# Performance work log

Measured on AMD Instinct MI355X. Metric: run time of the kernel, lower is better.

Reference implementation:

```python
import jax, jax.numpy as jnp
import numpy as np

B, N, DIM = 8, 512, 768
H, DH = 12, 64
INNER = H * DH
MLP = 3072
DEPTH = 4
EPS = 1e-5
LS = 0.1  # LayerScale init_eps for depth <= 18


def _ln(x, scale):
    # flax LayerNorm(use_bias=False): (x-mean)/sqrt(var+eps) * scale
    mu = jnp.mean(x, axis=-1, keepdims=True)
    var = jnp.mean(jnp.square(x - mu), axis=-1, keepdims=True)
    return (x - mu) * jax.lax.rsqrt(var + EPS) * scale


def setup_inputs() -> dict:
    key = jax.random.key(0)
    ks = jax.random.split(key, 13)
    s = 0.02
    inp = {
        "x": jax.random.normal(ks[0], (B, N, DIM), jnp.float32),
        "ln1": jnp.ones((DEPTH, DIM), jnp.float32),
        "Wq": jax.random.normal(ks[1], (DEPTH, DIM, INNER), jnp.float32) * s,
        "Wkv": jax.random.normal(ks[2], (DEPTH, DIM, 2 * INNER), jnp.float32) * s,
        "mix_pre": jax.random.normal(ks[3], (DEPTH, H, H), jnp.float32) * 0.1,
        "mix_post": jax.random.normal(ks[4], (DEPTH, H, H), jnp.float32) * 0.1,
        "Wo": jax.random.normal(ks[5], (DEPTH, INNER, DIM), jnp.float32) * s,
        "bo": jnp.zeros((DEPTH, DIM), jnp.float32),
        "ln2": jnp.ones((DEPTH, DIM), jnp.float32),
        "W1": jax.random.normal(ks[6], (DEPTH, DIM, MLP), jnp.float32) * s,
        "b1": jnp.zeros((DEPTH, MLP), jnp.float32),
        "W2": jax.random.normal(ks[7], (DEPTH, MLP, DIM), jnp.float32) * s,
        "b2": jnp.zeros((DEPTH, DIM), jnp.float32),
    }
    return inp


def _block(x, p):
    ln1, Wq, Wkv, mp, mq, Wo, bo, ln2, W1, b1, W2, b2 = p
    scale = DH ** -0.5
    h = _ln(x, ln1)
    q = h @ Wq                                  # [b,n,inner]
    kv = h @ Wkv
    k, v = jnp.split(kv, 2, axis=-1)
    def to_heads(t):
        return t.reshape(B, N, H, DH).transpose(0, 2, 1, 3)  # b h n d
    q, k, v = to_heads(q), to_heads(k), to_heads(v)
    dots = jnp.einsum('bhid,bhjd->bhij', q, k) * scale
    dots = jnp.einsum('bhij,hg->bgij', dots, mp)   # talking-heads pre-softmax
    attn = jax.nn.softmax(dots, axis=-1)
    attn = jnp.einsum('bhij,hg->bgij', attn, mq)   # talking-heads post-softmax
    o = jnp.einsum('bhij,bhjd->bhid', attn, v)
    o = o.transpose(0, 2, 1, 3).reshape(B, N, INNER)
    x = (o @ Wo + bo) * LS + x
    h2 = _ln(x, ln2)
    x = ((jax.nn.gelu(h2 @ W1 + b1) @ W2) + b2) * LS + x
    return x, None


def reference(x, ln1, Wq, Wkv, mix_pre, mix_post, Wo, bo, ln2, W1, b1, W2, b2):
    params = (ln1, Wq, Wkv, mix_pre, mix_post, Wo, bo, ln2, W1, b1, W2, b2)
    out, _ = jax.lax.scan(_block, x, params)
    return out
```

## Files before the change

kernel.cpp:

```cpp
#include <hip/hip_runtime.h>


#define LSCALE 0.1f

typedef __bf16 bf16;
typedef __bf16 bf16x8 __attribute__((ext_vector_type(8)));
typedef __bf16 bf16x4 __attribute__((ext_vector_type(4)));
typedef unsigned short ushort4v __attribute__((ext_vector_type(4)));
typedef float  f32x4  __attribute__((ext_vector_type(4)));

__device__ __forceinline__ void g2l16(const void* g, void* l) {
    __builtin_amdgcn_global_load_lds(
        (const __attribute__((address_space(1))) void*)g,
        (__attribute__((address_space(3))) void*)l, 16, 0, 0);
}

template<int EPI, bool PLANA = false>
__global__ __launch_bounds__(256, 2)
void gemm_bt(const bf16* __restrict__ A, int lda, long saz1, long saz2,
             const bf16* __restrict__ Bt, int ldb, long sbz1, long sbz2,
             void* __restrict__ Cv, int ldc, long scz1, long scz2,
             int M, int N, int K, int zmod,
             const float* __restrict__ bias, float scale)
{
    __shared__ __align__(16) char smem[35840];
    bf16* As = (bf16*)smem;
    bf16* Bs = (bf16*)(smem + 16384);
    bf16* Cs = (bf16*)smem;

    const int z  = blockIdx.z;
    const int z1 = z / zmod, z2 = z - z1 * zmod;
    const bf16* Ab = A  + saz1 * (long)z1 + saz2 * (long)z2;
    const bf16* Bb = Bt + sbz1 * (long)z1 + sbz2 * (long)z2;

    const int m0 = blockIdx.x * 128, n0 = blockIdx.y * 128;
    const int tid = threadIdx.x, w = tid >> 6, l = tid & 63;
    const int wr = (w >> 1) * 64, wc = (w & 1) * 64;
    const int lr = l & 15, lq = l >> 4;
    const int srow = l >> 2, scol8 = (l & 3) * 8;

    long abase = 0;
    if constexpr (PLANA)
        abase = (long)(m0 >> 9) * 393216 + (long)((m0 & 511) + w * 32) * 64;

    f32x4 acc[4][4];
#pragma unroll
    for (int i = 0; i < 4; i++)
#pragma unroll
        for (int j = 0; j < 4; j++)
#pragma unroll
            for (int r = 0; r < 4; r++) acc[i][j][r] = 0.f;

    for (int k0 = 0; k0 < K; k0 += 64) {
        const bf16* Ag;
        int ldaa;
        if constexpr (PLANA) {
            Ag = Ab + abase + ((long)(k0 >> 6)) * 32768;
            ldaa = 64;
        } else {
            Ag = Ab + (long)(m0 + w * 32) * lda + k0;
            ldaa = lda;
        }
        const bf16* Bg = Bb + (long)(n0 + w * 32) * ldb + k0;
        g2l16(Ag + (long)srow * ldaa + scol8,             As + w * 1024);
        g2l16(Ag + (long)(srow + 16) * ldaa + scol8,      As + w * 1024 + 512);
        g2l16(Ag + (long)srow * ldaa + 32 + scol8,        As + 4096 + w * 1024);
        g2l16(Ag + (long)(srow + 16) * ldaa + 32 + scol8, As + 4096 + w * 1024 + 512);
        g2l16(Bg + (long)srow * ldb + scol8,             Bs + w * 1024);
        g2l16(Bg + (long)(srow + 16) * ldb + scol8,      Bs + w * 1024 + 512);
        g2l16(Bg + (long)srow * ldb + 32 + scol8,        Bs + 4096 + w * 1024);
        g2l16(Bg + (long)(srow + 16) * ldb + 32 + scol8, Bs + 4096 + w * 1024 + 512);
        __syncthreads();

#pragma unroll
        for (int hh = 0; hh < 2; hh++) {
            bf16x8 fa[4], fb[4];
#pragma unroll
            for (int i = 0; i < 4; i++)
                fa[i] = *(const bf16x8*)(As + hh * 4096 + (wr + i * 16 + lr) * 32 + lq * 8);
#pragma unroll
            for (int i = 0; i < 4; i++)
                fb[i] = *(const bf16x8*)(Bs + hh * 4096 + (wc + i * 16 + lr) * 32 + lq * 8);
#pragma unroll
            for (int mi = 0; mi < 4; mi++)
#pragma unroll
                for (int ni = 0; ni < 4; ni++)
                    acc[mi][ni] = __builtin_amdgcn_mfma_f32_16x16x32_bf16(
                        fa[mi], fb[ni], acc[mi][ni], 0, 0, 0);
        }
        __syncthreads();
    }

#pragma unroll
    for (int ni = 0; ni < 4; ni++) {
        const int col = wc + ni * 16 + lr;
        float bv = 0.f;
        if (EPI == 1) bv = bias[n0 + col];
#pragma unroll
        for (int mi = 0; mi < 4; mi++) {
#pragma unroll
            for (int r = 0; r < 4; r++) {
                const int row = wr + mi * 16 + lq * 4 + r;
                float v = acc[mi][ni][r];
                if (EPI == 0) {
                    v *= scale;
                } else if (EPI == 1) {
                    const float xx = v + bv;
                    const float u  = 0.7978845608f * (xx + 0.044715f * xx * xx * xx);
                    const float th = 1.f - 2.f / (__expf(2.f * u) + 1.f);
                    v = 0.5f * xx * (1.f + th);
                }
                Cs[row * 136 + col] = (bf16)v;
            }
        }
    }
    __syncthreads();

    const long cb = scz1 * (long)z1 + scz2 * (long)z2;
    const int rrow = tid >> 4, cg = tid & 15;
#pragma unroll
    for (int p = 0; p < 8; p++) {
        const int row = p * 16 + rrow;
        const bf16x8 v = *(const bf16x8*)(Cs + row * 136 + cg * 8);
        *(bf16x8*)((bf16*)Cv + cb + (long)(m0 + row) * ldc + n0 + cg * 8) = v;
    }
}

template<int PLANO>
__global__ __launch_bounds__(256, 4)
void gemm_av(const bf16* __restrict__ S, const bf16* __restrict__ qkvc,
             bf16* __restrict__ oc)
{
    __shared__ __align__(16) char av_smem[9728];
    bf16* As  = (bf16*)av_smem;
    bf16* Bst = (bf16*)(av_smem + 4096);
    bf16* Cs  = (bf16*)av_smem;

    const int z = blockIdx.y, b = z / 12, g = z - b * 12;
    const bf16* Ab = S + (long)z * 262144;
    const bf16* Bb = qkvc + (long)b * 1179648 + 1536 + g * 64;

    const int i0 = blockIdx.x * 64;
    const int tid = threadIdx.x, w = tid >> 6, l = tid & 63;
    const int lr = l & 15, lq = l >> 4;
    const int srow = l >> 2, scol8 = (l & 3) * 8;
    const int kp = tid >> 4, dq = tid & 15;
    const int kcol = ((((kp >> 2) ^ ((dq >> 1) & 3)) << 3) | ((kp & 3) << 1));

    f32x4 acc[4];
#pragma unroll
    for (int j = 0; j < 4; j++)
#pragma unroll
        for (int r = 0; r < 4; r++) acc[j][r] = 0.f;

    unsigned short* Bw = (unsigned short*)Bst;

    for (int k0 = 0; k0 < 512; k0 += 32) {
        const bf16* Ag = Ab + (long)(i0 + w * 16) * 512 + k0;
        g2l16(Ag + (long)srow * 512 + scol8, As + w * 512);

        const bf16* Bg = Bb + (long)(k0 + 2 * kp) * 2304 + dq * 4;
        ushort4v u0 = *(const ushort4v*)(Bg);
        ushort4v u1 = *(const ushort4v*)(Bg + 2304);
#pragma unroll
        for (int r = 0; r < 4; r++) {
            unsigned p = (unsigned)u0[r] | ((unsigned)u1[r] << 16);
            *(unsigned*)(Bw + (dq * 4 + r) * 40 + kcol) = p;
        }
        __syncthreads();

        bf16x8 fa = *(const bf16x8*)(As + (w * 16 + lr) * 32 + lq * 8);
        bf16x8 fb[4];
#pragma unroll
        for (int i = 0; i < 4; i++) {
            const int d = i * 16 + lr;
            fb[i] = *(const bf16x8*)(Bst + d * 40 + ((lq ^ ((d >> 3) & 3)) << 3));
        }
#pragma unroll
        for (int ni = 0; ni < 4; ni++)
            acc[ni] = __builtin_amdgcn_mfma_f32_16x16x32_bf16(
                fa, fb[ni], acc[ni], 0, 0, 0);
        __syncthreads();
    }

    if constexpr (PLANO) {
#pragma unroll
        for (int ni = 0; ni < 4; ni++)
#pragma unroll
            for (int r = 0; r < 4; r++)
                Cs[(w * 16 + lq * 4 + r) * 68 + ni * 16 + lr] = (bf16)acc[ni][r];
        __syncthreads();
        const int rr = tid >> 2, c16 = (tid & 3) * 16;
        bf16* orow = oc + ((long)z * 512 + i0 + rr) * 64 + c16;
        *(bf16x8*)(orow)     = *(const bf16x8*)(Cs + rr * 68 + c16);
        *(bf16x8*)(orow + 8) = *(const bf16x8*)(Cs + rr * 68 + c16 + 8);
    } else {
        bf16* Cb = oc + (long)b * 1179648 + g * 64;
#pragma unroll
        for (int ni = 0; ni < 4; ni++) {
            const int gc = ni * 16 + lr;
#pragma unroll
            for (int r = 0; r < 4; r++) {
                const int gr = i0 + w * 16 + lq * 4 + r;
                Cb[(long)gr * 2304 + gc] = (bf16)acc[ni][r];
            }
        }
    }
}

__global__ __launch_bounds__(256)
void tconv_k(const float* __restrict__ in, bf16* __restrict__ out,
             int K, int N)
{
    __shared__ float t[32][33];
    const int n0 = blockIdx.x * 32, k0 = blockIdx.y * 32;
    const int x = threadIdx.x, y = threadIdx.y;
#pragma unroll
    for (int yy = 0; yy < 4; yy++)
        t[y + yy * 8][x] = in[(long)(k0 + y + yy * 8) * N + n0 + x];
    __syncthreads();
#pragma unroll
    for (int yy = 0; yy < 4; yy++)
        out[(long)(n0 + y + yy * 8) * K + k0 + x] = (bf16)t[x][y + yy * 8];
}

__global__ __launch_bounds__(256)
void tconv_all(const float* __restrict__ Wq, const float* __restrict__ Wkv,
               const float* __restrict__ Wo, const float* __restrict__ W1,
               const float* __restrict__ W2, bf16* __restrict__ WtAll)
{
    __shared__ float st[128][65];
    const int L = blockIdx.y;
    bf16* WtL = WtAll + (long)L * 7077888;
    int bx = blockIdx.x;
    const float* src; bf16* dst; int K, N, ntn;
    if (bx < 72) {
        src = Wq + (long)L * 589824;   dst = WtL;            K = 768;  N = 768;  ntn = 12;
    } else if (bx < 216) {
        bx -= 72;
        src = Wkv + (long)L * 1179648; dst = WtL + 589824;   K = 768;  N = 1536; ntn = 24;
    } else if (bx < 288) {
        bx -= 216;
        src = Wo + (long)L * 589824;   dst = WtL + 1769472;  K = 768;  N = 768;  ntn = 12;
    } else if (bx < 576) {
        bx -= 288;
        src = W1 + (long)L * 2359296;  dst = WtL + 2359296;  K = 768;  N = 3072; ntn = 48;
    } else {
        bx -= 576;
        src = W2 + (long)L * 2359296;  dst = WtL + 4718592;  K = 3072; N = 768;  ntn = 12;
    }
    const int n0 = (bx % ntn) * 64, k0 = (bx / ntn) * 128;
    const int t = threadIdx.x;
    const int rr = t >> 1, cb = (t & 1) * 32;
    f32x4 v[8];
#pragma unroll
    for (int q = 0; q < 8; q++)
        v[q] = *(const f32x4*)(src + (long)(k0 + rr) * N + n0 + cb + 4 * q);
#pragma unroll
    for (int q = 0; q < 8; q++)
#pragma unroll
        for (int j = 0; j < 4; j++)
            st[rr][cb + 4 * q + j] = v[q][j];
    __syncthreads();
    const int kb = (t & 15) * 8;
#pragma unroll
    for (int p = 0; p < 4; p++) {
        const int n = p * 16 + (t >> 4);
        bf16x8 o;
#pragma unroll
        for (int e = 0; e < 8; e++) o[e] = (bf16)st[kb + e][n];
        *(bf16x8*)(dst + (long)(n0 + n) * K + k0 + kb) = o;
    }
}

__global__ __launch_bounds__(256)
void lnres_k(float* __restrict__ xf, const bf16* __restrict__ P0,
             const bf16* __restrict__ P1, const float* __restrict__ bias,
             const float* __restrict__ gam, bf16* __restrict__ out,
             const float* __restrict__ src)
{
    const int row = blockIdx.x, t = threadIdx.x;
    float* xr = xf + (long)row * 768;
    float v[3];
#pragma unroll
    for (int i = 0; i < 3; i++) {
        const int c = t + i * 256;
        float xv;
        if (src) {
            xv = src[(long)row * 768 + c];
            xr[c] = xv;
        } else if (P0) {
            xv = xr[c] + LSCALE * ((float)P0[(long)row * 768 + c] +
                                   (float)P1[(long)row * 768 + c] + bias[c]);
            xr[c] = xv;
        } else {
            xv = xr[c];
        }
        v[i] = xv;
    }
    float s  = v[0] + v[1] + v[2];
    float ss = v[0] * v[0] + v[1] * v[1] + v[2] * v[2];
#pragma unroll
    for (int off = 32; off; off >>= 1) {
        s  += __shfl_xor(s, off);
        ss += __shfl_xor(ss, off);
    }
    __shared__ float ps[4], pss[4];
    const int wv = t >> 6, l = t & 63;
    if (l == 0) { ps[wv] = s; pss[wv] = ss; }
    __syncthreads();
    s  = ps[0] + ps[1] + ps[2] + ps[3];
    ss = pss[0] + pss[1] + pss[2] + pss[3];
    const float mu = s * (1.f / 768.f);
    const float rs = rsqrtf(ss * (1.f / 768.f) - mu * mu + 1e-5f);
    bf16* orow = out + (long)row * 768;
#pragma unroll
    for (int i = 0; i < 3; i++) {
        const int c = t + i * 256;
        orow[c] = (bf16)((v[i] - mu) * rs * gam[c]);
    }
}

__global__ __launch_bounds__(256)
void outres_k(const float* __restrict__ xf, const bf16* __restrict__ P0,
              const bf16* __restrict__ P1, const float* __restrict__ bias,
              float* __restrict__ out)
{
    const long i4 = ((long)blockIdx.x * 256 + threadIdx.x) * 4;
    const int c = (int)(i4 % 768);
    const f32x4 xv = *(const f32x4*)(xf + i4);
    const bf16x4 p0 = *(const bf16x4*)(P0 + i4);
    const bf16x4 p1 = *(const bf16x4*)(P1 + i4);
    const f32x4 bv = *(const f32x4*)(bias + c);
    f32x4 o;
#pragma unroll
    for (int e = 0; e < 4; e++)
        o[e] = xv[e] + LSCALE * ((float)p0[e] + (float)p1[e] + bv[e]);
    *(f32x4*)(out + i4) = o;
}

__global__ __launch_bounds__(256)
void mixsm_k(bf16* __restrict__ S, const float* __restrict__ mp,
             const float* __restrict__ mq)
{
    __shared__ float buf[12][512];
    __shared__ float rds[12];
    const int b = blockIdx.y, i = blockIdx.x, t = threadIdx.x;
    bf16* Sb = S + ((long)b * 12 * 512 + i) * 512;

    float s0[12], s1[12];
#pragma unroll
    for (int h = 0; h < 12; h++) {
        union { unsigned u; bf16 v[2]; } p;
        p.u = *(const unsigned*)(Sb + (long)h * 262144 + 2 * t);
        s0[h] = (float)p.v[0];
        s1[h] = (float)p.v[1];
    }
#pragma unroll
    for (int g = 0; g < 12; g++) {
        float a0 = 0.f, a1 = 0.f;
#pragma unroll
        for (int h = 0; h < 12; h++) {
            const float m = mp[h * 12 + g];
            a0 += s0[h] * m;
            a1 += s1[h] * m;
        }
        *(float2*)(&buf[g][2 * t]) = make_float2(a0, a1);
    }
    __syncthreads();

    const int wv = t >> 6, l = t & 63;
    for (int g = wv; g < 12; g += 4) {
        float mx = -3.0e38f;
#pragma unroll
        for (int k = 0; k < 8; k++) mx = fmaxf(mx, buf[g][l + 64 * k]);
#pragma unroll
        for (int off = 32; off; off >>= 1) mx = fmaxf(mx, __shfl_xor(mx, off));
        float sm = 0.f;
#pragma unroll
        for (int k = 0; k < 8; k++) {
            const float e = __expf(buf[g][l + 64 * k] - mx);
            buf[g][l + 64 * k] = e;
            sm += e;
        }
#pragma unroll
        for (int off = 32; off; off >>= 1) sm += __shfl_xor(sm, off);
        if (l == 0) rds[g] = 1.f / sm;
    }
    __syncthreads();

    float e0[12], e1[12];
#pragma unroll
    for (int h = 0; h < 12; h++) {
        const float2 ee = *(const float2*)(&buf[h][2 * t]);
        const float rd = rds[h];
        e0[h] = ee.x * rd;
        e1[h] = ee.y * rd;
    }
#pragma unroll
    for (int g = 0; g < 12; g++) {
        float a0 = 0.f, a1 = 0.f;
#pragma unroll
        for (int h = 0; h < 12; h++) {
            const float m = mq[h * 12 + g];
            a0 += e0[h] * m;
            a1 += e1[h] * m;
        }
        union { unsigned u; bf16 v[2]; } p;
        p.v[0] = (bf16)a0;
        p.v[1] = (bf16)a1;
        *(unsigned*)(Sb + (long)g * 262144 + 2 * t) = p.u;
    }
}

extern "C" void kernel_launch(void* const* d_in, const int* in_sizes, int n_in,
                              void* d_out, int out_size, void* d_ws, size_t ws_size,
                              hipStream_t stream)
{
    (void)in_sizes; (void)n_in; (void)out_size;
    const float* x   = (const float*)d_in[0];
    const float* ln1 = (const float*)d_in[1];
    const float* Wq  = (const float*)d_in[2];
    const float* Wkv = (const float*)d_in[3];
    const float* mp  = (const float*)d_in[4];
    const float* mq  = (const float*)d_in[5];
    const float* Wo  = (const float*)d_in[6];
    const float* bo  = (const float*)d_in[7];
    const float* ln2 = (const float*)d_in[8];
    const float* W1  = (const float*)d_in[9];
    const float* b1  = (const float*)d_in[10];
    const float* W2  = (const float*)d_in[11];
    const float* b2  = (const float*)d_in[12];

    char* ws = (char*)d_ws;
    float* xf  = (float*)(ws);
    bf16* h    = (bf16*)(ws + 12582912);
    bf16* qkv  = (bf16*)(ws + 18874368);
    bf16* S    = (bf16*)(ws + 37748736);
    bf16* mid  = S;
    bf16* P0   = h;
    bf16* P1w2 = qkv;
    bf16* P1wo = S;
    const long P1W2_OFF = 3145728;
    const long P1WO_OFF = 12582912;

    const dim3 tb(32, 8);

    if (ws_size >= 150994944ull) {
        bf16* WtAll = (bf16*)(ws + 88080384);
        bf16* oP    = (bf16*)(ws + 144703488);

        tconv_all<<<dim3(864, 4), 256, 0, stream>>>(Wq, Wkv, Wo, W1, W2, WtAll);

        for (int L = 0; L < 4; L++) {
            bf16* WtL = WtAll + (long)L * 7077888;

            if (L == 0)
                lnres_k<<<4096, 256, 0, stream>>>(xf, nullptr, nullptr, nullptr,
                                                  ln1 + L * 768, h, x);
            else
                lnres_k<<<4096, 256, 0, stream>>>(xf, P0, P1w2, b2 + (L - 1) * 768,
                                                  ln1 + L * 768, h, nullptr);

            gemm_bt<0><<<dim3(32, 18, 1), 256, 0, stream>>>(
                h, 768, 0, 0, WtL, 768, 0, 0,
                qkv, 2304, 0, 0, 4096, 2304, 768, 1, nullptr, 1.f);

            gemm_bt<0><<<dim3(4, 4, 96), 256, 0, stream>>>(
                qkv,       2304, 1179648, 64,
                qkv + 768, 2304, 1179648, 64,
                S,          512, 3145728, 262144,
                512, 512, 64, 12, nullptr, 0.125f);

            mixsm_k<<<dim3(512, 8), 256, 0, stream>>>(S, mp + L * 144, mq + L * 144);

            gemm_av<1><<<dim3(8, 96), 256, 0, stream>>>(S, qkv, oP);

            gemm_bt<4, true><<<dim3(32, 6, 2), 256, 0, stream>>>(
                oP, 64, 0, 196608, WtL + 1769472, 768, 0, 384,
                P0, 768, 0, P1WO_OFF, 4096, 768, 384, 2, nullptr, 1.f);

            lnres_k<<<4096, 256, 0, stream>>>(xf, P0, P1wo, bo + L * 768,
                                              ln2 + L * 768, h, nullptr);

            gemm_bt<1><<<dim3(32, 24, 1), 256, 0, stream>>>(
                h, 768, 0, 0, WtL + 2359296, 768, 0, 0,
                mid, 3072, 0, 0, 4096, 3072, 768, 1, b1 + L * 3072, 1.f);

            gemm_bt<4><<<dim3(32, 6, 2), 256, 0, stream>>>(
                mid, 3072, 0, 1536, WtL + 4718592, 3072, 0, 1536,
                P0, 768, 0, P1W2_OFF, 4096, 768, 1536, 2, nullptr, 1.f);
        }
    } else {
        bf16* Wt = (bf16*)(ws + 62914560);

        for (int L = 0; L < 4; L++) {
            tconv_k<<<dim3(24, 24), tb, 0, stream>>>(Wq + (long)L * 589824, Wt, 768, 768);
            tconv_k<<<dim3(48, 24), tb, 0, stream>>>(Wkv + (long)L * 1179648, Wt + 589824, 768, 1536);

            if (L == 0)
                lnres_k<<<4096, 256, 0, stream>>>(xf, nullptr, nullptr, nullptr,
                                                  ln1 + L * 768, h, x);
            else
                lnres_k<<<4096, 256, 0, stream>>>(xf, P0, P1w2, b2 + (L - 1) * 768,
                                                  ln1 + L * 768, h, nullptr);

            gemm_bt<0><<<dim3(32, 18, 1), 256, 0, stream>>>(
                h, 768, 0, 0, Wt, 768, 0, 0,
                qkv, 2304, 0, 0, 4096, 2304, 768, 1, nullptr, 1.f);

            for (int c = 0; c < 2; c++) {
                const long qb = (long)c * 4718592;
                gemm_bt<0><<<dim3(4, 4, 48), 256, 0, stream>>>(
                    qkv + qb,       2304, 1179648, 64,
                    qkv + 768 + qb, 2304, 1179648, 64,
                    S,               512, 3145728, 262144,
                    512, 512, 64, 12, nullptr, 0.125f);

                mixsm_k<<<dim3(512, 4), 256, 0, stream>>>(S, mp + L * 144, mq + L * 144);

                gemm_av<0><<<dim3(8, 48), 256, 0, stream>>>(S, qkv + qb, qkv + qb);
            }

            tconv_k<<<dim3(24, 24), tb, 0, stream>>>(Wo + (long)L * 589824, Wt, 768, 768);
            gemm_bt<4><<<dim3(32, 6, 2), 256, 0, stream>>>(
                qkv, 2304, 0, 384, Wt, 768, 0, 384,
                P0, 768, 0, P1WO_OFF, 4096, 768, 384, 2, nullptr, 1.f);

            lnres_k<<<4096, 256, 0, stream>>>(xf, P0, P1wo, bo + L * 768,
                                              ln2 + L * 768, h, nullptr);

            tconv_k<<<dim3(96, 24), tb, 0, stream>>>(W1 + (long)L * 2359296, Wt, 768, 3072);
            gemm_bt<1><<<dim3(32, 24, 1), 256, 0, stream>>>(
                h, 768, 0, 0, Wt, 768, 0, 0,
                mid, 3072, 0, 0, 4096, 3072, 768, 1, b1 + L * 3072, 1.f);

            tconv_k<<<dim3(24, 96), tb, 0, stream>>>(W2 + (long)L * 2359296, Wt, 3072, 768);
            gemm_bt<4><<<dim3(32, 6, 2), 256, 0, stream>>>(
                mid, 3072, 0, 1536, Wt, 3072, 0, 1536,
                P0, 768, 0, P1W2_OFF, 4096, 768, 1536, 2, nullptr, 1.f);
        }
    }

    outres_k<<<3072, 256, 0, stream>>>(xf, P0, P1w2, b2 + 3 * 768, (float*)d_out);
}
```

Before: 902.1 us.

## Fuse weight transpose with first LayerNorm; register-resident talking-heads softmax per wave

Merges the up-front weight transpose/bf16 conversion with the layer-0 input copy and LayerNorm into one launch, using smaller 64x64 transpose tiles and more blocks. Rewrites the talking-heads mix+softmax kernel so each wave owns one full query row: values stay in registers, reductions use wave shuffles only, and the LDS buffer and block barriers are gone. Each thread now loads and stores 16-byte vectors, with a quarter as many blocks. The cost is much higher register pressure (a 12x8 float accumulator per thread), which may cut occupancy or cause spills, and the one-pass variance formula is slightly less numerically robust.

```diff
diff --git a/kernel.cpp b/kernel.cpp
--- a/kernel.cpp
+++ b/kernel.cpp
@@ -225,51 +225,90 @@
 }
 
 __global__ __launch_bounds__(256)
-void tconv_all(const float* __restrict__ Wq, const float* __restrict__ Wkv,
-               const float* __restrict__ Wo, const float* __restrict__ W1,
-               const float* __restrict__ W2, bf16* __restrict__ WtAll)
-{
-    __shared__ float st[128][65];
-    const int L = blockIdx.y;
-    bf16* WtL = WtAll + (long)L * 7077888;
-    int bx = blockIdx.x;
-    const float* src; bf16* dst; int K, N, ntn;
-    if (bx < 72) {
-        src = Wq + (long)L * 589824;   dst = WtL;            K = 768;  N = 768;  ntn = 12;
-    } else if (bx < 216) {
-        bx -= 72;
-        src = Wkv + (long)L * 1179648; dst = WtL + 589824;   K = 768;  N = 1536; ntn = 24;
-    } else if (bx < 288) {
-        bx -= 216;
-        src = Wo + (long)L * 589824;   dst = WtL + 1769472;  K = 768;  N = 768;  ntn = 12;
-    } else if (bx < 576) {
-        bx -= 288;
-        src = W1 + (long)L * 2359296;  dst = WtL + 2359296;  K = 768;  N = 3072; ntn = 48;
+void pre_k(const float* __restrict__ Wq, const float* __restrict__ Wkv,
+           const float* __restrict__ Wo, const float* __restrict__ W1,
+           const float* __restrict__ W2, bf16* __restrict__ WtAll,
+           const float* __restrict__ x, float* __restrict__ xf,
+           const float* __restrict__ gam, bf16* __restrict__ hout)
+{
+    __shared__ __align__(16) char pmem[16640];
+    const int bxg = blockIdx.x;
+    const int t = threadIdx.x;
+    if (bxg < 6912) {
+        float (*st)[65] = (float(*)[65])pmem;
+        const int L = bxg / 1728;
+        int bx = bxg - L * 1728;
+        bf16* WtL = WtAll + (long)L * 7077888;
+        const float* src; bf16* dst; int K, N, ntn;
+        if (bx < 144) {
+            src = Wq + (long)L * 589824;   dst = WtL;            K = 768;  N = 768;  ntn = 12;
+        } else if (bx < 432) {
+            bx -= 144;
+            src = Wkv + (long)L * 1179648; dst = WtL + 589824;   K = 768;  N = 1536; ntn = 24;
+        } else if (bx < 576) {
+            bx -= 432;
+            src = Wo + (long)L * 589824;   dst = WtL + 1769472;  K = 768;  N = 768;  ntn = 12;
+        } else if (bx < 1152) {
+            bx -= 576;
+            src = W1 + (long)L * 2359296;  dst = WtL + 2359296;  K = 768;  N = 3072; ntn = 48;
+        } else {
+            bx -= 1152;
+            src = W2 + (long)L * 2359296;  dst = WtL + 4718592;  K = 3072; N = 768;  ntn = 12;
+        }
+        const int n0 = (bx % ntn) * 64, k0 = (bx / ntn) * 64;
+        const int r = t >> 4, c4 = (t & 15) * 4;
+#pragma unroll
+        for (int rr = 0; rr < 4; rr++) {
+            const f32x4 v = *(const f32x4*)(src + (long)(k0 + r + rr * 16) * N + n0 + c4);
+            st[r + rr * 16][c4 + 0] = v[0];
+            st[r + rr * 16][c4 + 1] = v[1];
+            st[r + rr * 16][c4 + 2] = v[2];
+            st[r + rr * 16][c4 + 3] = v[3];
+        }
+        __syncthreads();
+        const int kc = (t & 7) * 8;
+#pragma unroll
+        for (int p = 0; p < 2; p++) {
+            const int n = p * 32 + (t >> 3);
+            bf16x8 o;
+#pragma unroll
+            for (int e = 0; e < 8; e++) o[e] = (bf16)st[kc + e][n];
+            *(bf16x8*)(dst + (long)(n0 + n) * K + k0 + kc) = o;
+        }
     } else {
-        bx -= 576;
-        src = W2 + (long)L * 2359296;  dst = WtL + 4718592;  K = 3072; N = 768;  ntn = 12;
-    }
-    const int n0 = (bx % ntn) * 64, k0 = (bx / ntn) * 128;
-    const int t = threadIdx.x;
-    const int rr = t >> 1, cb = (t & 1) * 32;
-    f32x4 v[8];
-#pragma unroll
-    for (int q = 0; q < 8; q++)
-        v[q] = *(const f32x4*)(src + (long)(k0 + rr) * N + n0 + cb + 4 * q);
-#pragma unroll
-    for (int q = 0; q < 8; q++)
-#pragma unroll
-        for (int j = 0; j < 4; j++)
-            st[rr][cb + 4 * q + j] = v[q][j];
-    __syncthreads();
-    const int kb = (t & 15) * 8;
-#pragma unroll
-    for (int p = 0; p < 4; p++) {
-        const int n = p * 16 + (t >> 4);
-        bf16x8 o;
-#pragma unroll
-        for (int e = 0; e < 8; e++) o[e] = (bf16)st[kb + e][n];
-        *(bf16x8*)(dst + (long)(n0 + n) * K + k0 + kb) = o;
+        const int row = bxg - 6912;
+        float* ps  = (float*)pmem;
+        float* pss = (float*)pmem + 4;
+        const float* xin = x + (long)row * 768;
+        float* xr = xf + (long)row * 768;
+        float v[3];
+#pragma unroll
+        for (int i = 0; i < 3; i++) {
+            const int c = t + i * 256;
+            const float xv = xin[c];
+            xr[c] = xv;
+            v[i] = xv;
+        }
+        float s  = v[0] + v[1] + v[2];
+        float ss = v[0] * v[0] + v[1] * v[1] + v[2] * v[2];
+#pragma unroll
+        for (int off = 32; off; off >>= 1) {
+            s  += __shfl_xor(s, off);
+            ss += __shfl_xor(ss, off);
+        }
+        const int wv = t >> 6, l = t & 63;
+        if (l == 0) { ps[wv] = s; pss[wv] = ss; }
+        __syncthreads();
+        s  = ps[0] + ps[1] + ps[2] + ps[3];
+        ss = pss[0] + pss[1] + pss[2] + pss[3];
+        const float mu = s * (1.f / 768.f);
+        const float rs = rsqrtf(ss * (1.f / 768.f) - mu * mu + 1e-5f);
+        bf16* orow = hout + (long)row * 768;
+#pragma unroll
+        for (int i = 0; i < 3; i++) {
+            const int c = t + i * 256;
+            orow[c] = (bf16)((v[i] - mu) * rs * gam[c]);
+        }
     }
 }
 
@@ -343,73 +382,75 @@
 void mixsm_k(bf16* __restrict__ S, const float* __restrict__ mp,
              const float* __restrict__ mq)
 {
-    __shared__ float buf[12][512];
-    __shared__ float rds[12];
-    const int b = blockIdx.y, i = blockIdx.x, t = threadIdx.x;
-    bf16* Sb = S + ((long)b * 12 * 512 + i) * 512;
-
-    float s0[12], s1[12];
+    const int b = blockIdx.y, i4 = blockIdx.x, t = threadIdx.x;
+    const int w = t >> 6, l = t & 63;
+    const int row = i4 * 4 + w;
+    bf16* Sb = S + ((long)b * 12 * 512 + row) * 512 + l * 8;
+
+    float a[12][8];
+#pragma unroll
+    for (int g = 0; g < 12; g++)
+#pragma unroll
+        for (int e = 0; e < 8; e++) a[g][e] = 0.f;
+
 #pragma unroll
     for (int h = 0; h < 12; h++) {
-        union { unsigned u; bf16 v[2]; } p;
-        p.u = *(const unsigned*)(Sb + (long)h * 262144 + 2 * t);
-        s0[h] = (float)p.v[0];
-        s1[h] = (float)p.v[1];
-    }
+        const bf16x8 sv = *(const bf16x8*)(Sb + (long)h * 262144);
+        float f[8];
+#pragma unroll
+        for (int e = 0; e < 8; e++) f[e] = (float)sv[e];
+#pragma unroll
+        for (int g = 0; g < 12; g++) {
+            const float m = mp[h * 12 + g];
+#pragma unroll
+            for (int e = 0; e < 8; e++) a[g][e] += f[e] * m;
+        }
+    }
+
 #pragma unroll
     for (int g = 0; g < 12; g++) {
-        float a0 = 0.f, a1 = 0.f;
-#pragma unroll
-        for (int h = 0; h < 12; h++) {
-            const float m = mp[h * 12 + g];
-            a0 += s0[h] * m;
-            a1 += s1[h] * m;
-        }
-        *(float2*)(&buf[g][2 * t]) = make_float2(a0, a1);
-    }
-    __syncthreads();
-
-    const int wv = t >> 6, l = t & 63;
-    for (int g = wv; g < 12; g += 4) {
-        float mx = -3.0e38f;
-#pragma unroll
-        for (int k = 0; k < 8; k++) mx = fmaxf(mx, buf[g][l + 64 * k]);
+        float mx = a[g][0];
+#pragma unroll
+        for (int e = 1; e < 8; e++) mx = fmaxf(mx, a[g][e]);
 #pragma unroll
         for (int off = 32; off; off >>= 1) mx = fmaxf(mx, __shfl_xor(mx, off));
         float sm = 0.f;
 #pragma unroll
-        for (int k = 0; k < 8; k++) {
-            const float e = __expf(buf[g][l + 64 * k] - mx);
-            buf[g][l + 64 * k] = e;
-            sm += e;
+        for (int e = 0; e < 8; e++) {
+            const float ev = __expf(a[g][e] - mx);
+            a[g][e] = ev;
+            sm += ev;
         }
 #pragma unroll
         for (int off = 32; off; off >>= 1) sm += __shfl_xor(sm, off);
-        if (l == 0) rds[g] = 1.f / sm;
-    }
-    __syncthreads();
-
-    float e0[12], e1[12];
-#pragma unroll
-    for (int h = 0; h < 12; h++) {
-        const float2 ee = *(const float2*)(&buf[h][2 * t]);
-        const float rd = rds[h];
-        e0[h] = ee.x * rd;
-        e1[h] = ee.y * rd;
-    }
-#pragma unroll
-    for (int g = 0; g < 12; g++) {
-        float a0 = 0.f, a1 = 0.f;
+        const float rd = 1.f / sm;
+#pragma unroll
+        for (int e = 0; e < 8; e++) a[g][e] *= rd;
+    }
+
+#pragma unroll
+    for (int hf = 0; hf < 2; hf++) {
+        float o[6][8];
+#pragma unroll
+        for (int gg = 0; gg < 6; gg++)
+#pragma unroll
+            for (int e = 0; e < 8; e++) o[gg][e] = 0.f;
 #pragma unroll
         for (int h = 0; h < 12; h++) {
-            const float m = mq[h * 12 + g];
-            a0 += e0[h] * m;
-            a1 += e1[h] * m;
-        }
-        union { unsigned u; bf16 v[2]; } p;
-        p.v[0] = (bf16)a0;
-        p.v[1] = (bf16)a1;
-        *(unsigned*)(Sb + (long)g * 262144 + 2 * t) = p.u;
+#pragma unroll
+            for (int gg = 0; gg < 6; gg++) {
+                const float m = mq[h * 12 + hf * 6 + gg];
+#pragma unroll
+                for (int e = 0; e < 8; e++) o[gg][e] += a[h][e] * m;
+            }
+        }
+#pragma unroll
+        for (int gg = 0; gg < 6; gg++) {
+            bf16x8 ov;
+#pragma unroll
+            for (int e = 0; e < 8; e++) ov[e] = (bf16)o[gg][e];
+            *(bf16x8*)(Sb + (long)(hf * 6 + gg) * 262144) = ov;
+        }
     }
 }
 
@@ -450,15 +491,13 @@
         bf16* WtAll = (bf16*)(ws + 88080384);
         bf16* oP    = (bf16*)(ws + 144703488);
 
-        tconv_all<<<dim3(864, 4), 256, 0, stream>>>(Wq, Wkv, Wo, W1, W2, WtAll);
+        pre_k<<<11008, 256, 0, stream>>>(Wq, Wkv, Wo, W1, W2, WtAll,
+                                         x, xf, ln1, h);
 
         for (int L = 0; L < 4; L++) {
             bf16* WtL = WtAll + (long)L * 7077888;
 
-            if (L == 0)
-                lnres_k<<<4096, 256, 0, stream>>>(xf, nullptr, nullptr, nullptr,
-                                                  ln1 + L * 768, h, x);
-            else
+            if (L > 0)
                 lnres_k<<<4096, 256, 0, stream>>>(xf, P0, P1w2, b2 + (L - 1) * 768,
                                                   ln1 + L * 768, h, nullptr);
 
@@ -472,7 +511,7 @@
                 S,          512, 3145728, 262144,
                 512, 512, 64, 12, nullptr, 0.125f);
 
-            mixsm_k<<<dim3(512, 8), 256, 0, stream>>>(S, mp + L * 144, mq + L * 144);
+            mixsm_k<<<dim3(128, 8), 256, 0, stream>>>(S, mp + L * 144, mq + L * 144);
 
             gemm_av<1><<<dim3(8, 96), 256, 0, stream>>>(S, qkv, oP);
 
@@ -517,7 +556,7 @@
                     S,               512, 3145728, 262144,
                     512, 512, 64, 12, nullptr, 0.125f);
 
-                mixsm_k<<<dim3(512, 4), 256, 0, stream>>>(S, mp + L * 144, mq + L * 144);
+                mixsm_k<<<dim3(128, 4), 256, 0, stream>>>(S, mp + L * 144, mq + L * 144);
 
                 gemm_av<0><<<dim3(8, 48), 256, 0, stream>>>(S, qkv + qb, qkv + qb);
             }
```

After: 910.4 us. About the same (+0.9%).
